# Performance work log

Hardware: AMD Instinct MI355X
Metric: run time of the kernel (lower is better)

Reference implementation:

```python
import jax, jax.numpy as jnp
import numpy as np

B, T, S, H = 16, 1024, 2048, 1024


def setup_inputs() -> dict:
    key = jax.random.key(0)
    k1, k2, k3, k4, k5 = jax.random.split(key, 5)
    output = jax.random.normal(k1, (B, T, H), dtype=jnp.float32)
    context = jax.random.normal(k2, (B, S, H), dtype=jnp.float32)
    # nn.Linear(H, H, bias=False): weight [H, H], y = x @ W.T
    attn_weight = jax.random.normal(k3, (H, H), dtype=jnp.float32) * (1.0 / np.sqrt(H))
    # nn.Linear(2H, H): weight [H, 2H], bias [H]
    linear_out_w = jax.random.normal(k4, (H, 2 * H), dtype=jnp.float32) * (1.0 / np.sqrt(2 * H))
    linear_out_b = jax.random.normal(k5, (H,), dtype=jnp.float32) * 0.01
    return {"output": output, "context": context, "attn_weight": attn_weight,
            "linear_out_w": linear_out_w, "linear_out_b": linear_out_b}


def reference(output, context, attn_weight, linear_out_w, linear_out_b):
    # weighted query projection (use_weight=True)
    q = jnp.einsum('bth,oh->bto', output, attn_weight)  # [B,T,H]
    # scores + softmax over encoder positions
    attn = jax.nn.softmax(jnp.einsum('bth,bsh->bts', q, context), axis=-1)  # [B,T,S]
    mix = jnp.einsum('bts,bsh->bth', attn, context)  # [B,T,H]
    comb = jnp.concatenate([mix, q], axis=-1)  # [B,T,2H]
    out = jnp.tanh(jnp.einsum('btk,hk->bth', comb, linear_out_w) + linear_out_b)
    return (out, attn)
```

## Files before the change

### kernel.cpp

```cpp
#include <hip/hip_runtime.h>
#include <math.h>

typedef short bf16x8 __attribute__((ext_vector_type(8)));
typedef float f32x4 __attribute__((ext_vector_type(4)));
typedef unsigned short u16;

#define AS1 __attribute__((address_space(1)))
#define AS3 __attribute__((address_space(3)))

constexpr int kB = 16, kT = 1024, kS = 2048, kH = 1024;
constexpr long NTH = (long)kB * kT * kH;
constexpr long NSH = (long)kB * kS * kH;

__device__ __forceinline__ u16 bf16_rne(float x) {
    unsigned u = __float_as_uint(x);
    u += 0x7FFFu + ((u >> 16) & 1u);
    return (u16)(u >> 16);
}
__device__ __forceinline__ float bf16_f32(u16 h) {
    return __uint_as_float(((unsigned)h) << 16);
}
__device__ __forceinline__ void split2(float x, u16& hi, u16& lo) {
    hi = bf16_rne(x);
    lo = bf16_rne(x - bf16_f32(hi));
}

__device__ __forceinline__ void stage_gll(const u16* __restrict__ g, long ld, int t, u16* dst) {
    const int wave = t >> 6;
#pragma unroll
    for (int it = 0; it < 2; ++it) {
        const int u = it * 256 + t;
        const u16* src = g + (long)(u >> 2) * ld + ((u & 3) << 3);
        u16* l = dst + ((it << 2) + wave) * 512;
        __builtin_amdgcn_global_load_lds((AS1 void*)src, (AS3 void*)l, 16, 0, 0);
    }
}

__device__ __forceinline__ void mma_plain(const u16* As, const u16* Bs, f32x4 acc[4][4],
                                          int wr, int wc, int l15, int quad) {
    bf16x8 a[4], b[4];
#pragma unroll
    for (int i = 0; i < 4; ++i)
        a[i] = *(const bf16x8*)(As + (wr * 64 + i * 16 + l15) * 32 + quad * 8);
#pragma unroll
    for (int j = 0; j < 4; ++j)
        b[j] = *(const bf16x8*)(Bs + (wc * 64 + j * 16 + l15) * 32 + quad * 8);
#pragma unroll
    for (int i = 0; i < 4; ++i)
#pragma unroll
        for (int j = 0; j < 4; ++j)
            acc[i][j] = __builtin_amdgcn_mfma_f32_16x16x32_bf16(a[i], b[j], acc[i][j], 0, 0, 0);
}

__device__ __forceinline__ void mma_split(const u16* Ah, const u16* Al,
                                          const u16* Bh, const u16* Bl, f32x4 acc[4][4],
                                          int wr, int wc, int l15, int quad) {
    bf16x8 ah[4], al[4], bh[4], bl[4];
#pragma unroll
    for (int i = 0; i < 4; ++i) {
        int off = (wr * 64 + i * 16 + l15) * 32 + quad * 8;
        ah[i] = *(const bf16x8*)(Ah + off);
        al[i] = *(const bf16x8*)(Al + off);
    }
#pragma unroll
    for (int j = 0; j < 4; ++j) {
        int off = (wc * 64 + j * 16 + l15) * 32 + quad * 8;
        bh[j] = *(const bf16x8*)(Bh + off);
        bl[j] = *(const bf16x8*)(Bl + off);
    }
#pragma unroll
    for (int i = 0; i < 4; ++i)
#pragma unroll
        for (int j = 0; j < 4; ++j) {
            acc[i][j] = __builtin_amdgcn_mfma_f32_16x16x32_bf16(ah[i], bh[j], acc[i][j], 0, 0, 0);
            acc[i][j] = __builtin_amdgcn_mfma_f32_16x16x32_bf16(ah[i], bl[j], acc[i][j], 0, 0, 0);
            acc[i][j] = __builtin_amdgcn_mfma_f32_16x16x32_bf16(al[i], bh[j], acc[i][j], 0, 0, 0);
        }
}

__global__ __launch_bounds__(256) void split_f32(const float* __restrict__ src,
                                                 u16* __restrict__ hi, u16* __restrict__ lo,
                                                 long n4) {
    for (long i = (long)blockIdx.x * 256 + threadIdx.x; i < n4; i += (long)gridDim.x * 256) {
        float4 v = ((const float4*)src)[i];
        u16 h0, l0, h1, l1, h2, l2, h3, l3;
        split2(v.x, h0, l0); split2(v.y, h1, l1);
        split2(v.z, h2, l2); split2(v.w, h3, l3);
        ((ushort4*)hi)[i] = make_ushort4(h0, h1, h2, h3);
        ((ushort4*)lo)[i] = make_ushort4(l0, l1, l2, l3);
    }
}

__global__ __launch_bounds__(256) void cvt_f32(const float* __restrict__ src,
                                               u16* __restrict__ dst, long n4) {
    for (long i = (long)blockIdx.x * 256 + threadIdx.x; i < n4; i += (long)gridDim.x * 256) {
        float4 v = ((const float4*)src)[i];
        ((ushort4*)dst)[i] = make_ushort4(bf16_rne(v.x), bf16_rne(v.y),
                                          bf16_rne(v.z), bf16_rne(v.w));
    }
}

__global__ __launch_bounds__(256) void copy16(const uint4* __restrict__ src,
                                              uint4* __restrict__ dst, long n) {
    for (long i = (long)blockIdx.x * 256 + threadIdx.x; i < n; i += (long)gridDim.x * 256)
        dst[i] = src[i];
}

__global__ __launch_bounds__(256) void transpose_ctx(const float* __restrict__ ctx,
                                                     u16* __restrict__ ctxT) {
    __shared__ u16 tile[64 * 72];
    const int t = threadIdx.x;
    const float* src = ctx + (long)blockIdx.z * kS * kH + (long)(blockIdx.y * 64) * kH
                       + blockIdx.x * 64;
#pragma unroll
    for (int it = 0; it < 4; ++it) {
        int idx = it * 256 + t;
        int s = idx >> 4, hq = (idx & 15) << 2;
        float4 v = *(const float4*)(src + (long)s * kH + hq);
        tile[(hq + 0) * 72 + s] = bf16_rne(v.x);
        tile[(hq + 1) * 72 + s] = bf16_rne(v.y);
        tile[(hq + 2) * 72 + s] = bf16_rne(v.z);
        tile[(hq + 3) * 72 + s] = bf16_rne(v.w);
    }
    __syncthreads();
    u16* dst = ctxT + (long)blockIdx.z * kH * kS + (long)(blockIdx.x * 64) * kS
               + blockIdx.y * 64;
#pragma unroll
    for (int it = 0; it < 2; ++it) {
        int idx = it * 256 + t;
        int h = idx >> 3, sq = (idx & 7) << 3;
        *(uint4*)(dst + (long)h * kS + sq) = *(const uint4*)&tile[h * 72 + sq];
    }
}

__global__ __launch_bounds__(256) void gemm_q(const u16* __restrict__ Ahg,
                                              const u16* __restrict__ Alg,
                                              const u16* __restrict__ Bhg,
                                              const u16* __restrict__ Blg,
                                              u16* __restrict__ Qhi, u16* __restrict__ Qlo) {
    __shared__ u16 Ah[128 * 32], Al[128 * 32], Bh[128 * 32], Bl[128 * 32];
    const int t = threadIdx.x, lane = t & 63, wave = t >> 6;
    const int wr = wave >> 1, wc = wave & 1, l15 = lane & 15, quad = lane >> 4;
    const long bm = blockIdx.y * 128, bn = blockIdx.x * 128;

    f32x4 acc[4][4] = {};
    for (int k0 = 0; k0 < kH; k0 += 32) {
        stage_gll(Ahg + bm * kH + k0, kH, t, Ah);
        stage_gll(Alg + bm * kH + k0, kH, t, Al);
        stage_gll(Bhg + bn * kH + k0, kH, t, Bh);
        stage_gll(Blg + bn * kH + k0, kH, t, Bl);
        __syncthreads();
        mma_split(Ah, Al, Bh, Bl, acc, wr, wc, l15, quad);
        __syncthreads();
    }
#pragma unroll
    for (int i = 0; i < 4; ++i)
#pragma unroll
        for (int j = 0; j < 4; ++j)
#pragma unroll
            for (int r = 0; r < 4; ++r) {
                long m = bm + wr * 64 + i * 16 + quad * 4 + r;
                long n = bn + wc * 64 + j * 16 + l15;
                float v = acc[i][j][r];
                u16 h = bf16_rne(v);
                Qhi[m * kH + n] = h;
                Qlo[m * kH + n] = bf16_rne(v - bf16_f32(h));
            }
}

__global__ __launch_bounds__(256) void gemm_logits(const u16* __restrict__ Qhi,
                                                   const u16* __restrict__ Qlo,
                                                   const u16* __restrict__ Chi,
                                                   const u16* __restrict__ Clo,
                                                   float* __restrict__ Cout) {
    __shared__ u16 Ah[128 * 32], Al[128 * 32], Bh[128 * 32], Bl[128 * 32];
    const int t = threadIdx.x, lane = t & 63, wave = t >> 6;
    const int wr = wave >> 1, wc = wave & 1, l15 = lane & 15, quad = lane >> 4;
    const int z = blockIdx.z;
    const long bm = blockIdx.y * 128, bn = blockIdx.x * 128;
    const u16* qh = Qhi + (long)z * kT * kH;
    const u16* ql = Qlo + (long)z * kT * kH;
    const u16* ch = Chi + (long)z * kS * kH;
    const u16* cl = Clo + (long)z * kS * kH;
    float* C = Cout + (long)z * kT * kS;

    f32x4 acc[4][4] = {};
    for (int k0 = 0; k0 < kH; k0 += 32) {
        stage_gll(qh + bm * kH + k0, kH, t, Ah);
        stage_gll(ql + bm * kH + k0, kH, t, Al);
        stage_gll(ch + bn * kH + k0, kH, t, Bh);
        stage_gll(cl + bn * kH + k0, kH, t, Bl);
        __syncthreads();
        mma_split(Ah, Al, Bh, Bl, acc, wr, wc, l15, quad);
        __syncthreads();
    }
#pragma unroll
    for (int i = 0; i < 4; ++i)
#pragma unroll
        for (int j = 0; j < 4; ++j)
#pragma unroll
            for (int r = 0; r < 4; ++r) {
                long m = bm + wr * 64 + i * 16 + quad * 4 + r;
                long n = bn + wc * 64 + j * 16 + l15;
                C[m * kS + n] = acc[i][j][r];
            }
}

__global__ __launch_bounds__(256) void softmax_rows(float* __restrict__ P,
                                                    u16* __restrict__ Pb) {
    __shared__ float red[4];
    float* p = P + (long)blockIdx.x * kS;
    u16* pb = Pb + (long)blockIdx.x * kS;
    const int t = threadIdx.x;

    float4 v0 = ((const float4*)p)[t];
    float4 v1 = ((const float4*)p)[t + 256];

    float m = fmaxf(fmaxf(fmaxf(v0.x, v0.y), fmaxf(v0.z, v0.w)),
                    fmaxf(fmaxf(v1.x, v1.y), fmaxf(v1.z, v1.w)));
#pragma unroll
    for (int o = 32; o > 0; o >>= 1) m = fmaxf(m, __shfl_xor(m, o));
    if ((t & 63) == 0) red[t >> 6] = m;
    __syncthreads();
    m = fmaxf(fmaxf(red[0], red[1]), fmaxf(red[2], red[3]));
    __syncthreads();

    v0.x = expf(v0.x - m); v0.y = expf(v0.y - m);
    v0.z = expf(v0.z - m); v0.w = expf(v0.w - m);
    v1.x = expf(v1.x - m); v1.y = expf(v1.y - m);
    v1.z = expf(v1.z - m); v1.w = expf(v1.w - m);

    float s = v0.x + v0.y + v0.z + v0.w + v1.x + v1.y + v1.z + v1.w;
#pragma unroll
    for (int o = 32; o > 0; o >>= 1) s += __shfl_xor(s, o);
    if ((t & 63) == 0) red[t >> 6] = s;
    __syncthreads();
    s = red[0] + red[1] + red[2] + red[3];

    const float inv = 1.0f / s;
    v0.x *= inv; v0.y *= inv; v0.z *= inv; v0.w *= inv;
    v1.x *= inv; v1.y *= inv; v1.z *= inv; v1.w *= inv;

    ((float4*)p)[t]       = v0;
    ((float4*)p)[t + 256] = v1;
    ((ushort4*)pb)[t]       = make_ushort4(bf16_rne(v0.x), bf16_rne(v0.y),
                                           bf16_rne(v0.z), bf16_rne(v0.w));
    ((ushort4*)pb)[t + 256] = make_ushort4(bf16_rne(v1.x), bf16_rne(v1.y),
                                           bf16_rne(v1.z), bf16_rne(v1.w));
}

__global__ __launch_bounds__(256) void gemm_mix(const u16* __restrict__ attnb,
                                                const u16* __restrict__ ctxT,
                                                u16* __restrict__ Mixb) {
    __shared__ u16 As[128 * 32], Bs[128 * 32];
    const int t = threadIdx.x, lane = t & 63, wave = t >> 6;
    const int wr = wave >> 1, wc = wave & 1, l15 = lane & 15, quad = lane >> 4;
    const int z = blockIdx.z;
    const long bm = blockIdx.y * 128, bn = blockIdx.x * 128;
    const u16* Ab = attnb + (long)z * kT * kS;
    const u16* Bb = ctxT + (long)z * kH * kS;
    u16* C = Mixb + (long)z * kT * kH;

    f32x4 acc[4][4] = {};
    for (int k0 = 0; k0 < kS; k0 += 32) {
        stage_gll(Ab + bm * kS + k0, kS, t, As);
        stage_gll(Bb + bn * kS + k0, kS, t, Bs);
        __syncthreads();
        mma_plain(As, Bs, acc, wr, wc, l15, quad);
        __syncthreads();
    }
#pragma unroll
    for (int i = 0; i < 4; ++i)
#pragma unroll
        for (int j = 0; j < 4; ++j)
#pragma unroll
            for (int r = 0; r < 4; ++r) {
                long m = bm + wr * 64 + i * 16 + quad * 4 + r;
                long n = bn + wc * 64 + j * 16 + l15;
                C[m * kH + n] = bf16_rne(acc[i][j][r]);
            }
}

__global__ __launch_bounds__(256) void gemm_out(const u16* __restrict__ Mixc,
                                                const u16* __restrict__ Qc,
                                                const u16* __restrict__ Wb,
                                                const float* __restrict__ bias,
                                                float* __restrict__ Out) {
    __shared__ u16 As[128 * 32], Bs[128 * 32];
    const int t = threadIdx.x, lane = t & 63, wave = t >> 6;
    const int wr = wave >> 1, wc = wave & 1, l15 = lane & 15, quad = lane >> 4;
    const long bm = blockIdx.y * 128, bn = blockIdx.x * 128;

    f32x4 acc[4][4] = {};
    for (int k0 = 0; k0 < 2 * kH; k0 += 32) {
        const u16* Ab = (k0 < kH) ? (Mixc + bm * kH + k0) : (Qc + bm * kH + (k0 - kH));
        stage_gll(Ab, kH, t, As);
        stage_gll(Wb + bn * (2 * kH) + k0, 2 * kH, t, Bs);
        __syncthreads();
        mma_plain(As, Bs, acc, wr, wc, l15, quad);
        __syncthreads();
    }
#pragma unroll
    for (int j = 0; j < 4; ++j) {
        long n = bn + wc * 64 + j * 16 + l15;
        float bj = bias[n];
#pragma unroll
        for (int i = 0; i < 4; ++i)
#pragma unroll
            for (int r = 0; r < 4; ++r) {
                long m = bm + wr * 64 + i * 16 + quad * 4 + r;
                Out[m * kH + n] = tanhf(acc[i][j][r] + bj);
            }
    }
}

extern "C" void kernel_launch(void* const* d_in, const int* in_sizes, int n_in,
                              void* d_out, int out_size, void* d_ws, size_t ws_size,
                              hipStream_t stream) {
    (void)in_sizes; (void)n_in; (void)out_size; (void)ws_size;

    const float* outp = (const float*)d_in[0];
    const float* ctx  = (const float*)d_in[1];
    const float* aw   = (const float*)d_in[2];
    const float* lw   = (const float*)d_in[3];
    const float* lb   = (const float*)d_in[4];

    float* out  = (float*)d_out;
    float* attn = out + NTH;

    u16* ws = (u16*)d_ws;
    u16* ctx_hi = ws;
    u16* ctx_lo = ws + NSH;
    u16* q_hi = (u16*)out;
    u16* q_lo = q_hi + NTH;
    u16* oh  = (u16*)attn;
    u16* ol  = oh + NTH;
    u16* awh = ol + NTH;
    u16* awl = awh + (long)kH * kH;
    u16* ctxT  = ws;
    u16* attnb = ws + NSH;
    u16* mixb  = q_lo;
    u16* q_c   = ws;
    u16* mix_c = ws + NTH;
    u16* lwb   = ws + 2 * NTH;

    split_f32<<<2048, 256, 0, stream>>>(ctx, ctx_hi, ctx_lo, NSH / 4);
    split_f32<<<2048, 256, 0, stream>>>(outp, oh, ol, NTH / 4);
    split_f32<<<1024, 256, 0, stream>>>(aw, awh, awl, (long)kH * kH / 4);

    gemm_q<<<dim3(kH / 128, (kB * kT) / 128), 256, 0, stream>>>(oh, ol, awh, awl, q_hi, q_lo);
    gemm_logits<<<dim3(kS / 128, kT / 128, kB), 256, 0, stream>>>(q_hi, q_lo, ctx_hi, ctx_lo,
                                                                  attn);
    softmax_rows<<<kB * kT, 256, 0, stream>>>(attn, attnb);
    transpose_ctx<<<dim3(kH / 64, kS / 64, kB), 256, 0, stream>>>(ctx, ctxT);
    gemm_mix<<<dim3(kH / 128, kT / 128, kB), 256, 0, stream>>>(attnb, ctxT, mixb);

    copy16<<<2048, 256, 0, stream>>>((const uint4*)q_hi, (uint4*)ws, (2 * NTH) / 8);
    cvt_f32<<<2048, 256, 0, stream>>>(lw, lwb, (long)kH * 2 * kH / 4);

    gemm_out<<<dim3(kH / 128, (kB * kT) / 128), 256, 0, stream>>>(mix_c, q_c, lwb, lb, out);
}
```

Measured before the change: 1.019 ms.

## Rewrite GEMMs with 256x256 double-buffered swizzled tiles and XCD-aware block mapping

```diff
diff --git a/kernel.cpp b/kernel.cpp
--- a/kernel.cpp
+++ b/kernel.cpp
@@ -25,57 +25,224 @@
     lo = bf16_rne(x - bf16_f32(hi));
 }
 
-__device__ __forceinline__ void stage_gll(const u16* __restrict__ g, long ld, int t, u16* dst) {
-    const int wave = t >> 6;
-#pragma unroll
-    for (int it = 0; it < 2; ++it) {
-        const int u = it * 256 + t;
-        const u16* src = g + (long)(u >> 2) * ld + ((u & 3) << 3);
-        u16* l = dst + ((it << 2) + wave) * 512;
-        __builtin_amdgcn_global_load_lds((AS1 void*)src, (AS3 void*)l, 16, 0, 0);
-    }
-}
-
-__device__ __forceinline__ void mma_plain(const u16* As, const u16* Bs, f32x4 acc[4][4],
-                                          int wr, int wc, int l15, int quad) {
-    bf16x8 a[4], b[4];
-#pragma unroll
-    for (int i = 0; i < 4; ++i)
-        a[i] = *(const bf16x8*)(As + (wr * 64 + i * 16 + l15) * 32 + quad * 8);
-#pragma unroll
-    for (int j = 0; j < 4; ++j)
-        b[j] = *(const bf16x8*)(Bs + (wc * 64 + j * 16 + l15) * 32 + quad * 8);
-#pragma unroll
-    for (int i = 0; i < 4; ++i)
+
+__device__ __forceinline__ void stage_mat(const u16* __restrict__ g, long ld,
+                                          u16* lds, int t, int wave) {
+#pragma unroll
+    for (int c = 0; c < 4; ++c) {
+        int u = c * 512 + t;
+        int r = u >> 3, j = u & 7;
+        const u16* src = g + (long)r * ld + ((j ^ (r & 7)) << 3);
+        u16* dst = lds + c * 4096 + wave * 512;
+        __builtin_amdgcn_global_load_lds((AS1 void*)src, (AS3 void*)dst, 16, 0, 0);
+    }
+}
+
+__device__ __forceinline__ void tile_compute(const u16* As, const u16* Bs,
+                                             f32x4 acc[8][4], int wr, int wc,
+                                             int l15, int cbu0, int cbu1) {
+    bf16x8 b[4][2];
+#pragma unroll
+    for (int j = 0; j < 4; ++j) {
+        const u16* base = Bs + (wc * 64 + j * 16 + l15) * 64;
+        b[j][0] = *(const bf16x8*)(base + cbu0);
+        b[j][1] = *(const bf16x8*)(base + cbu1);
+    }
+#pragma unroll
+    for (int qm = 0; qm < 2; ++qm) {
+        bf16x8 a[4][2];
+#pragma unroll
+        for (int i = 0; i < 4; ++i) {
+            const u16* base = As + (wr * 128 + qm * 64 + i * 16 + l15) * 64;
+            a[i][0] = *(const bf16x8*)(base + cbu0);
+            a[i][1] = *(const bf16x8*)(base + cbu1);
+        }
+        __builtin_amdgcn_s_setprio(1);
+#pragma unroll
+        for (int i = 0; i < 4; ++i)
+#pragma unroll
+            for (int j = 0; j < 4; ++j) {
+                acc[qm * 4 + i][j] = __builtin_amdgcn_mfma_f32_16x16x32_bf16(
+                    a[i][0], b[j][0], acc[qm * 4 + i][j], 0, 0, 0);
+                acc[qm * 4 + i][j] = __builtin_amdgcn_mfma_f32_16x16x32_bf16(
+                    a[i][1], b[j][1], acc[qm * 4 + i][j], 0, 0, 0);
+            }
+        __builtin_amdgcn_s_setprio(0);
+    }
+}
+
+#define WAIT_VM(N)                                            \
+    asm volatile("s_waitcnt vmcnt(" #N ")" ::: "memory");     \
+    __builtin_amdgcn_s_barrier();                             \
+    __builtin_amdgcn_sched_barrier(0);
+
+#define POST_BARRIER()                                        \
+    __builtin_amdgcn_sched_barrier(0);                        \
+    __builtin_amdgcn_s_barrier();                             \
+    __builtin_amdgcn_sched_barrier(0);
+
+template <int NT, int TPS>
+__device__ __forceinline__ void gemm_core(const u16* a0, const u16* a1, const u16* a2,
+                                          long lda,
+                                          const u16* b0, const u16* b1, const u16* b2,
+                                          long ldb, f32x4 acc[8][4]) {
+    __shared__ u16 As[2][256 * 64], Bs[2][256 * 64];
+    const int t = threadIdx.x, lane = t & 63, wave = t >> 6;
+    const int wr = wave >> 2, wc = wave & 3, l15 = lane & 15, quad = lane >> 4;
+    const int swzb = (l15 & 7) << 4;
+    const int cbu0 = ((quad * 16) ^ swzb) >> 1;
+    const int cbu1 = ((quad * 16 + 64) ^ swzb) >> 1;
+
+    auto srcA = [&](int kt) {
+        int seg = kt / TPS;
+        const u16* p = (seg == 0) ? a0 : (seg == 1 ? a1 : a2);
+        return p + (long)(kt % TPS) * 64;
+    };
+    auto srcB = [&](int kt) {
+        int seg = kt / TPS;
+        const u16* p = (seg == 0) ? b0 : (seg == 1 ? b1 : b2);
+        return p + (long)(kt % TPS) * 64;
+    };
+
+    stage_mat(srcA(0), lda, As[0], t, wave);
+    stage_mat(srcB(0), ldb, Bs[0], t, wave);
+    __builtin_amdgcn_sched_barrier(0);
+    stage_mat(srcA(1), lda, As[1], t, wave);
+    stage_mat(srcB(1), ldb, Bs[1], t, wave);
+    __builtin_amdgcn_sched_barrier(0);
+
+#pragma unroll 1
+    for (int it = 0; it < NT / 2 - 1; ++it) {
+        int kt = 2 * it;
+        WAIT_VM(8)
+        tile_compute(As[0], Bs[0], acc, wr, wc, l15, cbu0, cbu1);
+        POST_BARRIER()
+        stage_mat(srcA(kt + 2), lda, As[0], t, wave);
+        stage_mat(srcB(kt + 2), ldb, Bs[0], t, wave);
+
+        WAIT_VM(8)
+        tile_compute(As[1], Bs[1], acc, wr, wc, l15, cbu0, cbu1);
+        POST_BARRIER()
+        stage_mat(srcA(kt + 3), lda, As[1], t, wave);
+        stage_mat(srcB(kt + 3), ldb, Bs[1], t, wave);
+    }
+    WAIT_VM(8)
+    tile_compute(As[0], Bs[0], acc, wr, wc, l15, cbu0, cbu1);
+    WAIT_VM(0)
+    tile_compute(As[1], Bs[1], acc, wr, wc, l15, cbu0, cbu1);
+}
+
+__global__ __launch_bounds__(512, 2) void k_gemm_q(const u16* __restrict__ oh,
+                                                   const u16* __restrict__ ol,
+                                                   const u16* __restrict__ awh,
+                                                   const u16* __restrict__ awl,
+                                                   u16* __restrict__ Qhi,
+                                                   u16* __restrict__ Qlo) {
+    const long bm = (long)blockIdx.y * 256, bn = (long)blockIdx.x * 256;
+    f32x4 acc[8][4] = {};
+    gemm_core<48, 16>(oh + bm * kH, ol + bm * kH, oh + bm * kH, kH,
+                      awh + bn * kH, awh + bn * kH, awl + bn * kH, kH, acc);
+    const int t = threadIdx.x, lane = t & 63, wave = t >> 6;
+    const int wr = wave >> 2, wc = wave & 3, l15 = lane & 15, quad = lane >> 4;
+#pragma unroll
+    for (int i = 0; i < 8; ++i)
 #pragma unroll
         for (int j = 0; j < 4; ++j)
-            acc[i][j] = __builtin_amdgcn_mfma_f32_16x16x32_bf16(a[i], b[j], acc[i][j], 0, 0, 0);
-}
-
-__device__ __forceinline__ void mma_split(const u16* Ah, const u16* Al,
-                                          const u16* Bh, const u16* Bl, f32x4 acc[4][4],
-                                          int wr, int wc, int l15, int quad) {
-    bf16x8 ah[4], al[4], bh[4], bl[4];
-#pragma unroll
-    for (int i = 0; i < 4; ++i) {
-        int off = (wr * 64 + i * 16 + l15) * 32 + quad * 8;
-        ah[i] = *(const bf16x8*)(Ah + off);
-        al[i] = *(const bf16x8*)(Al + off);
-    }
+#pragma unroll
+            for (int r = 0; r < 4; ++r) {
+                long m = bm + wr * 128 + i * 16 + quad * 4 + r;
+                long n = bn + wc * 64 + j * 16 + l15;
+                float v = acc[i][j][r];
+                u16 h = bf16_rne(v);
+                Qhi[m * kH + n] = h;
+                Qlo[m * kH + n] = bf16_rne(v - bf16_f32(h));
+            }
+}
+
+__global__ __launch_bounds__(512, 2) void k_gemm_logits(const u16* __restrict__ Qh,
+                                                        const u16* __restrict__ Ql,
+                                                        const u16* __restrict__ Ch,
+                                                        const u16* __restrict__ Cl,
+                                                        float* __restrict__ Cout) {
+    const int l = blockIdx.x;
+    const int xcd = l & 7, slot = l >> 3;
+    const int z = xcd + ((slot >> 5) << 3);
+    const int inner = slot & 31;
+    const long bn = (long)(inner & 7) * 256;
+    const long bm = (long)(inner >> 3) * 256;
+    const u16* qh = Qh + (long)z * kT * kH + bm * kH;
+    const u16* ql = Ql + (long)z * kT * kH + bm * kH;
+    const u16* ch = Ch + (long)z * kS * kH + bn * kH;
+    const u16* cl = Cl + (long)z * kS * kH + bn * kH;
+    f32x4 acc[8][4] = {};
+    gemm_core<48, 16>(qh, ql, qh, kH, ch, ch, cl, kH, acc);
+    float* C = Cout + (long)z * kT * kS;
+    const int t = threadIdx.x, lane = t & 63, wave = t >> 6;
+    const int wr = wave >> 2, wc = wave & 3, l15 = lane & 15, quad = lane >> 4;
+#pragma unroll
+    for (int i = 0; i < 8; ++i)
+#pragma unroll
+        for (int j = 0; j < 4; ++j)
+#pragma unroll
+            for (int r = 0; r < 4; ++r) {
+                long m = bm + wr * 128 + i * 16 + quad * 4 + r;
+                long n = bn + wc * 64 + j * 16 + l15;
+                C[m * kS + n] = acc[i][j][r];
+            }
+}
+
+__global__ __launch_bounds__(512, 2) void k_gemm_mix(const u16* __restrict__ attnb,
+                                                     const u16* __restrict__ ctxT,
+                                                     u16* __restrict__ Mixb) {
+    const int l = blockIdx.x;
+    const int xcd = l & 7, slot = l >> 3;
+    const int z = xcd + ((slot >> 4) << 3);
+    const int inner = slot & 15;
+    const long bn = (long)(inner & 3) * 256;
+    const long bm = (long)(inner >> 2) * 256;
+    const u16* Ab = attnb + (long)z * kT * kS + bm * kS;
+    const u16* Bb = ctxT + (long)z * kH * kS + bn * kS;
+    f32x4 acc[8][4] = {};
+    gemm_core<32, 32>(Ab, Ab, Ab, kS, Bb, Bb, Bb, kS, acc);
+    u16* C = Mixb + (long)z * kT * kH;
+    const int t = threadIdx.x, lane = t & 63, wave = t >> 6;
+    const int wr = wave >> 2, wc = wave & 3, l15 = lane & 15, quad = lane >> 4;
+#pragma unroll
+    for (int i = 0; i < 8; ++i)
+#pragma unroll
+        for (int j = 0; j < 4; ++j)
+#pragma unroll
+            for (int r = 0; r < 4; ++r) {
+                long m = bm + wr * 128 + i * 16 + quad * 4 + r;
+                long n = bn + wc * 64 + j * 16 + l15;
+                C[m * kH + n] = bf16_rne(acc[i][j][r]);
+            }
+}
+
+__global__ __launch_bounds__(512, 2) void k_gemm_out(const u16* __restrict__ mixc,
+                                                     const u16* __restrict__ qc,
+                                                     const u16* __restrict__ lwb,
+                                                     const float* __restrict__ bias,
+                                                     float* __restrict__ Out) {
+    const long bm = (long)blockIdx.y * 256, bn = (long)blockIdx.x * 256;
+    f32x4 acc[8][4] = {};
+    gemm_core<32, 16>(mixc + bm * kH, qc + bm * kH, qc + bm * kH, kH,
+                      lwb + bn * 2 * kH, lwb + bn * 2 * kH + kH, lwb + bn * 2 * kH + kH,
+                      2 * kH, acc);
+    const int t = threadIdx.x, lane = t & 63, wave = t >> 6;
+    const int wr = wave >> 2, wc = wave & 3, l15 = lane & 15, quad = lane >> 4;
 #pragma unroll
     for (int j = 0; j < 4; ++j) {
-        int off = (wc * 64 + j * 16 + l15) * 32 + quad * 8;
-        bh[j] = *(const bf16x8*)(Bh + off);
-        bl[j] = *(const bf16x8*)(Bl + off);
-    }
-#pragma unroll
-    for (int i = 0; i < 4; ++i)
-#pragma unroll
-        for (int j = 0; j < 4; ++j) {
-            acc[i][j] = __builtin_amdgcn_mfma_f32_16x16x32_bf16(ah[i], bh[j], acc[i][j], 0, 0, 0);
-            acc[i][j] = __builtin_amdgcn_mfma_f32_16x16x32_bf16(ah[i], bl[j], acc[i][j], 0, 0, 0);
-            acc[i][j] = __builtin_amdgcn_mfma_f32_16x16x32_bf16(al[i], bh[j], acc[i][j], 0, 0, 0);
-        }
+        long n = bn + wc * 64 + j * 16 + l15;
+        float bj = bias[n];
+#pragma unroll
+        for (int i = 0; i < 8; ++i)
+#pragma unroll
+            for (int r = 0; r < 4; ++r) {
+                long m = bm + wr * 128 + i * 16 + quad * 4 + r;
+                Out[m * kH + n] = tanhf(acc[i][j][r] + bj);
+            }
+    }
 }
 
 __global__ __launch_bounds__(256) void split_f32(const float* __restrict__ src,
@@ -106,104 +273,30 @@
         dst[i] = src[i];
 }
 
-__global__ __launch_bounds__(256) void transpose_ctx(const float* __restrict__ ctx,
-                                                     u16* __restrict__ ctxT) {
+__global__ __launch_bounds__(256) void transpose_bf16(const u16* __restrict__ in,
+                                                      u16* __restrict__ outp) {
     __shared__ u16 tile[64 * 72];
     const int t = threadIdx.x;
-    const float* src = ctx + (long)blockIdx.z * kS * kH + (long)(blockIdx.y * 64) * kH
-                       + blockIdx.x * 64;
-#pragma unroll
-    for (int it = 0; it < 4; ++it) {
-        int idx = it * 256 + t;
-        int s = idx >> 4, hq = (idx & 15) << 2;
-        float4 v = *(const float4*)(src + (long)s * kH + hq);
-        tile[(hq + 0) * 72 + s] = bf16_rne(v.x);
-        tile[(hq + 1) * 72 + s] = bf16_rne(v.y);
-        tile[(hq + 2) * 72 + s] = bf16_rne(v.z);
-        tile[(hq + 3) * 72 + s] = bf16_rne(v.w);
-    }
-    __syncthreads();
-    u16* dst = ctxT + (long)blockIdx.z * kH * kS + (long)(blockIdx.x * 64) * kS
-               + blockIdx.y * 64;
+    const u16* src = in + (long)blockIdx.z * kS * kH + (long)(blockIdx.y * 64) * kH
+                     + blockIdx.x * 64;
 #pragma unroll
     for (int it = 0; it < 2; ++it) {
         int idx = it * 256 + t;
-        int h = idx >> 3, sq = (idx & 7) << 3;
-        *(uint4*)(dst + (long)h * kS + sq) = *(const uint4*)&tile[h * 72 + sq];
-    }
-}
-
-__global__ __launch_bounds__(256) void gemm_q(const u16* __restrict__ Ahg,
-                                              const u16* __restrict__ Alg,
-                                              const u16* __restrict__ Bhg,
-                                              const u16* __restrict__ Blg,
-                                              u16* __restrict__ Qhi, u16* __restrict__ Qlo) {
-    __shared__ u16 Ah[128 * 32], Al[128 * 32], Bh[128 * 32], Bl[128 * 32];
-    const int t = threadIdx.x, lane = t & 63, wave = t >> 6;
-    const int wr = wave >> 1, wc = wave & 1, l15 = lane & 15, quad = lane >> 4;
-    const long bm = blockIdx.y * 128, bn = blockIdx.x * 128;
-
-    f32x4 acc[4][4] = {};
-    for (int k0 = 0; k0 < kH; k0 += 32) {
-        stage_gll(Ahg + bm * kH + k0, kH, t, Ah);
-        stage_gll(Alg + bm * kH + k0, kH, t, Al);
-        stage_gll(Bhg + bn * kH + k0, kH, t, Bh);
-        stage_gll(Blg + bn * kH + k0, kH, t, Bl);
-        __syncthreads();
-        mma_split(Ah, Al, Bh, Bl, acc, wr, wc, l15, quad);
-        __syncthreads();
-    }
-#pragma unroll
-    for (int i = 0; i < 4; ++i)
-#pragma unroll
-        for (int j = 0; j < 4; ++j)
-#pragma unroll
-            for (int r = 0; r < 4; ++r) {
-                long m = bm + wr * 64 + i * 16 + quad * 4 + r;
-                long n = bn + wc * 64 + j * 16 + l15;
-                float v = acc[i][j][r];
-                u16 h = bf16_rne(v);
-                Qhi[m * kH + n] = h;
-                Qlo[m * kH + n] = bf16_rne(v - bf16_f32(h));
-            }
-}
-
-__global__ __launch_bounds__(256) void gemm_logits(const u16* __restrict__ Qhi,
-                                                   const u16* __restrict__ Qlo,
-                                                   const u16* __restrict__ Chi,
-                                                   const u16* __restrict__ Clo,
-                                                   float* __restrict__ Cout) {
-    __shared__ u16 Ah[128 * 32], Al[128 * 32], Bh[128 * 32], Bl[128 * 32];
-    const int t = threadIdx.x, lane = t & 63, wave = t >> 6;
-    const int wr = wave >> 1, wc = wave & 1, l15 = lane & 15, quad = lane >> 4;
-    const int z = blockIdx.z;
-    const long bm = blockIdx.y * 128, bn = blockIdx.x * 128;
-    const u16* qh = Qhi + (long)z * kT * kH;
-    const u16* ql = Qlo + (long)z * kT * kH;
-    const u16* ch = Chi + (long)z * kS * kH;
-    const u16* cl = Clo + (long)z * kS * kH;
-    float* C = Cout + (long)z * kT * kS;
-
-    f32x4 acc[4][4] = {};
-    for (int k0 = 0; k0 < kH; k0 += 32) {
-        stage_gll(qh + bm * kH + k0, kH, t, Ah);
-        stage_gll(ql + bm * kH + k0, kH, t, Al);
-        stage_gll(ch + bn * kH + k0, kH, t, Bh);
-        stage_gll(cl + bn * kH + k0, kH, t, Bl);
-        __syncthreads();
-        mma_split(Ah, Al, Bh, Bl, acc, wr, wc, l15, quad);
-        __syncthreads();
-    }
-#pragma unroll
-    for (int i = 0; i < 4; ++i)
-#pragma unroll
-        for (int j = 0; j < 4; ++j)
-#pragma unroll
-            for (int r = 0; r < 4; ++r) {
-                long m = bm + wr * 64 + i * 16 + quad * 4 + r;
-                long n = bn + wc * 64 + j * 16 + l15;
-                C[m * kS + n] = acc[i][j][r];
-            }
+        int s = idx >> 3, hc = (idx & 7) << 3;
+        uint4 v = *(const uint4*)(src + (long)s * kH + hc);
+        const u16* pv = (const u16*)&v;
+#pragma unroll
+        for (int k = 0; k < 8; ++k) tile[(hc + k) * 72 + s] = pv[k];
+    }
+    __syncthreads();
+    u16* dst = outp + (long)blockIdx.z * kH * kS + (long)(blockIdx.x * 64) * kS
+               + blockIdx.y * 64;
+#pragma unroll
+    for (int it = 0; it < 2; ++it) {
+        int idx = it * 256 + t;
+        int h = idx >> 3, sc = (idx & 7) << 3;
+        *(uint4*)(dst + (long)h * kS + sc) = *(const uint4*)&tile[h * 72 + sc];
+    }
 }
 
 __global__ __launch_bounds__(256) void softmax_rows(float* __restrict__ P,
@@ -247,71 +340,6 @@
                                            bf16_rne(v0.z), bf16_rne(v0.w));
     ((ushort4*)pb)[t + 256] = make_ushort4(bf16_rne(v1.x), bf16_rne(v1.y),
                                            bf16_rne(v1.z), bf16_rne(v1.w));
-}
-
-__global__ __launch_bounds__(256) void gemm_mix(const u16* __restrict__ attnb,
-                                                const u16* __restrict__ ctxT,
-                                                u16* __restrict__ Mixb) {
-    __shared__ u16 As[128 * 32], Bs[128 * 32];
-    const int t = threadIdx.x, lane = t & 63, wave = t >> 6;
-    const int wr = wave >> 1, wc = wave & 1, l15 = lane & 15, quad = lane >> 4;
-    const int z = blockIdx.z;
-    const long bm = blockIdx.y * 128, bn = blockIdx.x * 128;
-    const u16* Ab = attnb + (long)z * kT * kS;
-    const u16* Bb = ctxT + (long)z * kH * kS;
-    u16* C = Mixb + (long)z * kT * kH;
-
-    f32x4 acc[4][4] = {};
-    for (int k0 = 0; k0 < kS; k0 += 32) {
-        stage_gll(Ab + bm * kS + k0, kS, t, As);
-        stage_gll(Bb + bn * kS + k0, kS, t, Bs);
-        __syncthreads();
-        mma_plain(As, Bs, acc, wr, wc, l15, quad);
-        __syncthreads();
-    }
-#pragma unroll
-    for (int i = 0; i < 4; ++i)
-#pragma unroll
-        for (int j = 0; j < 4; ++j)
-#pragma unroll
-            for (int r = 0; r < 4; ++r) {
-                long m = bm + wr * 64 + i * 16 + quad * 4 + r;
-                long n = bn + wc * 64 + j * 16 + l15;
-                C[m * kH + n] = bf16_rne(acc[i][j][r]);
-            }
-}
-
-__global__ __launch_bounds__(256) void gemm_out(const u16* __restrict__ Mixc,
-                                                const u16* __restrict__ Qc,
-                                                const u16* __restrict__ Wb,
-                                                const float* __restrict__ bias,
-                                                float* __restrict__ Out) {
-    __shared__ u16 As[128 * 32], Bs[128 * 32];
-    const int t = threadIdx.x, lane = t & 63, wave = t >> 6;
-    const int wr = wave >> 1, wc = wave & 1, l15 = lane & 15, quad = lane >> 4;
-    const long bm = blockIdx.y * 128, bn = blockIdx.x * 128;
-
-    f32x4 acc[4][4] = {};
-    for (int k0 = 0; k0 < 2 * kH; k0 += 32) {
-        const u16* Ab = (k0 < kH) ? (Mixc + bm * kH + k0) : (Qc + bm * kH + (k0 - kH));
-        stage_gll(Ab, kH, t, As);
-        stage_gll(Wb + bn * (2 * kH) + k0, 2 * kH, t, Bs);
-        __syncthreads();
-        mma_plain(As, Bs, acc, wr, wc, l15, quad);
-        __syncthreads();
-    }
-#pragma unroll
-    for (int j = 0; j < 4; ++j) {
-        long n = bn + wc * 64 + j * 16 + l15;
-        float bj = bias[n];
-#pragma unroll
-        for (int i = 0; i < 4; ++i)
-#pragma unroll
-            for (int r = 0; r < 4; ++r) {
-                long m = bm + wr * 64 + i * 16 + quad * 4 + r;
-                Out[m * kH + n] = tanhf(acc[i][j][r] + bj);
-            }
-    }
 }
 
 extern "C" void kernel_launch(void* const* d_in, const int* in_sizes, int n_in,
@@ -337,8 +365,8 @@
     u16* ol  = oh + NTH;
     u16* awh = ol + NTH;
     u16* awl = awh + (long)kH * kH;
-    u16* ctxT  = ws;
-    u16* attnb = ws + NSH;
+    u16* ctxT  = ws + NSH;
+    u16* attnb = ws;
     u16* mixb  = q_lo;
     u16* q_c   = ws;
     u16* mix_c = ws + NTH;
@@ -348,15 +376,17 @@
     split_f32<<<2048, 256, 0, stream>>>(outp, oh, ol, NTH / 4);
     split_f32<<<1024, 256, 0, stream>>>(aw, awh, awl, (long)kH * kH / 4);
 
-    gemm_q<<<dim3(kH / 128, (kB * kT) / 128), 256, 0, stream>>>(oh, ol, awh, awl, q_hi, q_lo);
-    gemm_logits<<<dim3(kS / 128, kT / 128, kB), 256, 0, stream>>>(q_hi, q_lo, ctx_hi, ctx_lo,
-                                                                  attn);
+    k_gemm_q<<<dim3(kH / 256, (kB * kT) / 256), 512, 0, stream>>>(oh, ol, awh, awl,
+                                                                  q_hi, q_lo);
+    k_gemm_logits<<<512, 512, 0, stream>>>(q_hi, q_lo, ctx_hi, ctx_lo, attn);
+
+    transpose_bf16<<<dim3(kH / 64, kS / 64, kB), 256, 0, stream>>>(ctx_hi, ctxT);
     softmax_rows<<<kB * kT, 256, 0, stream>>>(attn, attnb);
-    transpose_ctx<<<dim3(kH / 64, kS / 64, kB), 256, 0, stream>>>(ctx, ctxT);
-    gemm_mix<<<dim3(kH / 128, kT / 128, kB), 256, 0, stream>>>(attnb, ctxT, mixb);
+
+    k_gemm_mix<<<256, 512, 0, stream>>>(attnb, ctxT, mixb);
 
     copy16<<<2048, 256, 0, stream>>>((const uint4*)q_hi, (uint4*)ws, (2 * NTH) / 8);
     cvt_f32<<<2048, 256, 0, stream>>>(lw, lwb, (long)kH * 2 * kH / 4);
 
-    gemm_out<<<dim3(kH / 128, (kB * kT) / 128), 256, 0, stream>>>(mix_c, q_c, lwb, lb, out);
-}
+    k_gemm_out<<<dim3(kH / 256, (kB * kT) / 256), 512, 0, stream>>>(mix_c, q_c, lwb, lb, out);
+}
```

New measurement: 891.3 us. -12.5%, faster.
